# Kernel tuning notes

Hardware: AMD Instinct MI355X
Metric: run time of the kernel (lower is better)

The kernel has to match this reference:

```python
import jax, jax.numpy as jnp
import numpy as np


def setup_inputs() -> dict:
    key = jax.random.key(0)
    k1, k2 = jax.random.split(key)
    B, T, D = 8, 2048, 2048
    layer_in = jax.random.normal(k1, (B, T, D), dtype=jnp.float32)
    # nn.Linear(2D, 2D): weight [out=2D, in=2D], bias [2D]
    W_gate = jax.random.normal(k2, (2 * D, 2 * D), dtype=jnp.float32) * 0.02
    b_gate = jnp.zeros((2 * D,), dtype=jnp.float32)
    return {"layer_in": layer_in, "W_gate": W_gate, "b_gate": b_gate}


def reference(layer_in, W_gate, b_gate):
    # Cumulative average: tril(ones)/row_index @ x  ==  cumsum(x)/[1..t]
    t = layer_in.shape[1]
    denom = jnp.arange(1, t + 1, dtype=layer_in.dtype)[:, None]  # (t, 1)
    average_out = jnp.cumsum(layer_in, axis=1) / denom  # (B, t, D)
    # Gating: Linear(2D -> 2D) on concat(x, avg), then chunk into two gates
    gating_in = jnp.concatenate([layer_in, average_out], axis=-1)  # (B, t, 2D)
    gates = jnp.einsum('btk,ok->bto', gating_in, W_gate) + b_gate  # (B, t, 2D)
    input_gate, forget_gate = jnp.split(gates, 2, axis=2)
    gating_out = (jax.nn.sigmoid(input_gate) * layer_in
                  + jax.nn.sigmoid(forget_gate) * average_out)
    return gating_out, average_out
```

## Files before the change

### kernel.cpp

```cpp
#include <hip/hip_runtime.h>
#include <hip/hip_bf16.h>


#define Bb 8
#define Tt 2048
#define Dd 2048
#define Mm (Bb * Tt)
#define Kk 4096
#define NC 32
#define CT 64

typedef __bf16 bf16x8 __attribute__((ext_vector_type(8)));
typedef float f32x4 __attribute__((ext_vector_type(4)));

__device__ __forceinline__ void gload16(const void* g, void* l) {
    __builtin_amdgcn_global_load_lds(
        (const __attribute__((address_space(1))) unsigned int*)g,
        (__attribute__((address_space(3))) unsigned int*)l, 16, 0, 0);
}

__global__ void wconv_kernel(const float* __restrict__ W,
                             unsigned short* __restrict__ Wb, long n) {
    long i = ((long)blockIdx.x * blockDim.x + threadIdx.x) * 4;
    long stride = (long)gridDim.x * blockDim.x * 4;
    for (; i < n; i += stride) {
        float4 v = *(const float4*)(W + i);
        __hip_bfloat16 a = __float2bfloat16(v.x);
        __hip_bfloat16 b = __float2bfloat16(v.y);
        __hip_bfloat16 c = __float2bfloat16(v.z);
        __hip_bfloat16 d = __float2bfloat16(v.w);
        ushort4 u;
        u.x = *(unsigned short*)&a; u.y = *(unsigned short*)&b;
        u.z = *(unsigned short*)&c; u.w = *(unsigned short*)&d;
        *(ushort4*)(Wb + i) = u;
    }
}

__global__ void ksum_kernel(const float* __restrict__ X, float* __restrict__ S,
                            unsigned short* __restrict__ Gin) {
    int d = blockIdx.y * 256 + threadIdx.x;
    int bc = blockIdx.x;
    int b = bc >> 5, c = bc & 31;
    const float* p = X + ((long)(b * Tt + c * CT)) * Dd + d;
    long row = (long)b * Tt + c * CT;
    float s = 0.f;
#pragma unroll 8
    for (int t = 0; t < CT; ++t) {
        float x = p[(long)t * Dd];
        s += x;
        __hip_bfloat16 xb = __float2bfloat16(x);
        Gin[(row + t) * 4096 + d] = *(unsigned short*)&xb;
    }
    S[(long)bc * Dd + d] = s;
}

__global__ void kscan_kernel(const unsigned short* __restrict__ Ginx,
                             const float* __restrict__ S,
                             float* __restrict__ AVG, unsigned short* __restrict__ Gin) {
    int d = blockIdx.y * 256 + threadIdx.x;
    int bc = blockIdx.x;
    int b = bc >> 5, c = bc & 31;
    const float* Sp = S + (long)(b * NC) * Dd + d;
    float run = 0.f;
    for (int cc = 0; cc < c; ++cc) run += Sp[(long)cc * Dd];
    long row = (long)b * Tt + c * CT;
    for (int tt = 0; tt < CT; ++tt) {
        long r = row + tt;
        union { unsigned int u; float f; } cx;
        cx.u = ((unsigned int)Ginx[r * 4096 + d]) << 16;
        run += cx.f;
        float av = run / (float)(c * CT + tt + 1);
        AVG[r * Dd + d] = av;
        __hip_bfloat16 ab = __float2bfloat16(av);
        Gin[r * 4096 + 2048 + d] = *(unsigned short*)&ab;
    }
}

#define MFMA(va, vb, c_) c_ = __builtin_amdgcn_mfma_f32_16x16x32_bf16(va, vb, c_, 0, 0, 0)
#define RD(p_, i_) (*(const bf16x8*)((p_) + (i_) * 1024))
#define SBAR __builtin_amdgcn_s_barrier()
#define SCHB __builtin_amdgcn_sched_barrier(0)
#define LGKM0 do { asm volatile("s_waitcnt lgkmcnt(0)" ::: "memory"); SCHB; } while (0)

#define CL_LO(B0_, B1_, B2_, B3_)                                               \
    __builtin_amdgcn_s_setprio(1);                                              \
    MFMA(aL0,B0_,acc[0][0]); MFMA(aL0,B1_,acc[0][1]); MFMA(aL0,B2_,acc[0][2]); MFMA(aL0,B3_,acc[0][3]); \
    MFMA(aL1,B0_,acc[1][0]); MFMA(aL1,B1_,acc[1][1]); MFMA(aL1,B2_,acc[1][2]); MFMA(aL1,B3_,acc[1][3]); \
    MFMA(aL2,B0_,acc[2][0]); MFMA(aL2,B1_,acc[2][1]); MFMA(aL2,B2_,acc[2][2]); MFMA(aL2,B3_,acc[2][3]); \
    MFMA(aL3,B0_,acc[3][0]); MFMA(aL3,B1_,acc[3][1]); MFMA(aL3,B2_,acc[3][2]); MFMA(aL3,B3_,acc[3][3]); \
    __builtin_amdgcn_s_setprio(0);
#define CL_HI(B0_, B1_, B2_, B3_)                                               \
    __builtin_amdgcn_s_setprio(1);                                              \
    MFMA(aH0,B0_,acc[4][0]); MFMA(aH0,B1_,acc[4][1]); MFMA(aH0,B2_,acc[4][2]); MFMA(aH0,B3_,acc[4][3]); \
    MFMA(aH1,B0_,acc[5][0]); MFMA(aH1,B1_,acc[5][1]); MFMA(aH1,B2_,acc[5][2]); MFMA(aH1,B3_,acc[5][3]); \
    MFMA(aH2,B0_,acc[6][0]); MFMA(aH2,B1_,acc[6][1]); MFMA(aH2,B2_,acc[6][2]); MFMA(aH2,B3_,acc[6][3]); \
    MFMA(aH3,B0_,acc[7][0]); MFMA(aH3,B1_,acc[7][1]); MFMA(aH3,B2_,acc[7][2]); MFMA(aH3,B3_,acc[7][3]); \
    __builtin_amdgcn_s_setprio(0);

#define TILE64(t_, bb_, STG_, VB_)                                              \
  {                                                                             \
    const char* pa_ = rA0 + (bb_);                                              \
    const char* pb_ = rB0 + (bb_);                                              \
    char* nb_ = ldsb + ((bb_) ^ 65536) + woff;                                  \
    const long ko_ = ((long)(t_) + 1) * 128;                                    \
                                \
    aL0 = RD(pa_,0); aL1 = RD(pa_,1); aL2 = RD(pa_,2); aL3 = RD(pa_,3);         \
    bb0 = RD(pb_,0); bb1 = RD(pb_,1); bb2 = RD(pb_,2); bb3 = RD(pb_,3);         \
    if (STG_) { gload16(gA0 + ko_, nb_); gload16(gA1 + ko_, nb_ + 8192); }      \
    LGKM0;                                                         \
                                      \
    aH0 = RD(pa_,4); aH1 = RD(pa_,5); aH2 = RD(pa_,6); aH3 = RD(pa_,7);         \
    SCHB;                                                                       \
    CL_LO(bb0, bb1, bb2, bb3)                                                   \
    SCHB;                                                                       \
    LGKM0;                                                         \
             \
    aL0 = RD(pa_+32768,0); aL1 = RD(pa_+32768,1); aL2 = RD(pa_+32768,2); aL3 = RD(pa_+32768,3); \
    bd0 = RD(pb_+32768,0); bd1 = RD(pb_+32768,1); bd2 = RD(pb_+32768,2); bd3 = RD(pb_+32768,3); \
    if (STG_) { gload16(gB0 + ko_, nb_ + 16384); gload16(gB1 + ko_, nb_ + 24576); } \
    SCHB;                                                                       \
    CL_HI(bb0, bb1, bb2, bb3)                                                   \
    SCHB;                                                                       \
    LGKM0;                                                         \
                     \
    aH0 = RD(pa_+32768,4); aH1 = RD(pa_+32768,5); aH2 = RD(pa_+32768,6); aH3 = RD(pa_+32768,7); \
    if (STG_) { gload16(gA0 + ko_ + 64, nb_ + 32768); gload16(gA1 + ko_ + 64, nb_ + 40960); } \
    SCHB;                                                                       \
    CL_LO(bd0, bd1, bd2, bd3)                                                   \
    SCHB;                                                                       \
    LGKM0;                                                         \
                                         \
    if (STG_) { gload16(gB0 + ko_ + 64, nb_ + 49152); gload16(gB1 + ko_ + 64, nb_ + 57344); } \
    SCHB;                                                                       \
    CL_HI(bd0, bd1, bd2, bd3)                                                   \
    SCHB;                                                                       \
    asm volatile("s_waitcnt vmcnt(" #VB_ ")" ::: "memory");                     \
    SBAR; SCHB;                                          \
  }

__global__ __launch_bounds__(512, 1) void gemmcf_kernel(
    const unsigned short* __restrict__ Gin,
    const unsigned short* __restrict__ Wb,
    const float* __restrict__ bias,
    float* __restrict__ OUT)
{
    __shared__ __attribute__((aligned(128))) char lds[131072];
    char* ldsb = (char*)lds;

    const int tid = threadIdx.x;
    const int w = tid >> 6, l = tid & 63;
    const int wm = w >> 2, wn = w & 3;
    const int lm = l & 15;
    const int woff = w * 1024;

    const int bid = blockIdx.x;
    const int batch = bid >> 8;
    const int rr = bid & 255;
    const int xcd = rr & 7;
    const int j = rr >> 3;
    const int nt = xcd * 2 + (j >> 4);
    const int mt = batch * 16 + (j & 15);
    const long m0 = (long)mt * 256;
    const int n0 = nt * 128;

    const int srow = tid >> 2;
    const int schunk = (tid & 3) ^ ((tid >> 3) & 3);
    const char* gA0 = (const char*)Gin + (m0 + srow) * 8192 + schunk * 16;
    const char* gA1 = gA0 + 128 * 8192;
    const long jr0 = n0 + ((srow >> 6) << 5) + (srow & 31) + (((srow >> 5) & 1) << 11);
    const int j1 = 128 + srow;
    const long jr1 = n0 + ((j1 >> 6) << 5) + (j1 & 31) + (((j1 >> 5) & 1) << 11);
    const char* gB0 = (const char*)Wb + jr0 * 8192 + schunk * 16;
    const char* gB1 = (const char*)Wb + jr1 * 8192 + schunk * 16;

    const int cbyte = (((l >> 4) ^ ((lm >> 1) & 3))) * 16;
    const char* rA0 = ldsb + (wm * 128 + lm) * 64 + cbyte;
    const char* rB0 = ldsb + 16384 + (wn * 64 + lm) * 64 + cbyte;

    f32x4 acc[8][4] = {};

    bf16x8 aL0, aL1, aL2, aL3, aH0, aH1, aH2, aH3;
    bf16x8 bb0, bb1, bb2, bb3, bd0, bd1, bd2, bd3;

    gload16(gA0,      ldsb + woff);
    gload16(gA1,      ldsb + 8192 + woff);
    gload16(gB0,      ldsb + 16384 + woff);
    gload16(gB1,      ldsb + 24576 + woff);
    gload16(gA0 + 64, ldsb + 32768 + woff);
    gload16(gA1 + 64, ldsb + 40960 + woff);
    gload16(gB0 + 64, ldsb + 49152 + woff);
    gload16(gB1 + 64, ldsb + 57344 + woff);
    asm volatile("s_waitcnt vmcnt(0)" ::: "memory");
    SBAR; SCHB;

#pragma unroll 1
    for (int t = 0; t < 62; t += 2) {
        TILE64(t,     0,     1, 0)
        TILE64(t + 1, 65536, 1, 0)
    }
    TILE64(62, 0,     1, 0)
    TILE64(63, 65536, 0, 0)

#pragma unroll
    for (int mi = 0; mi < 8; ++mi) {
        long rbase = m0 + wm * 128 + mi * 16 + (l >> 4) * 4;
#pragma unroll
        for (int nj = 0; nj < 2; ++nj) {
            int d = n0 + wn * 32 + nj * 16 + lm;
            float bi_ = bias[d];
            float bf_ = bias[d + 2048];
#pragma unroll
            for (int r = 0; r < 4; ++r) {
                long row = rbase + r;
                unsigned int ux = Gin[row * 4096 + d];
                unsigned int ua = Gin[row * 4096 + 2048 + d];
                union { unsigned int u; float f; } cx, ca;
                cx.u = ux << 16; ca.u = ua << 16;
                float gi = acc[mi][nj][r] + bi_;
                float gf = acc[mi][nj + 2][r] + bf_;
                float si = 1.f / (1.f + __expf(-gi));
                float sf = 1.f / (1.f + __expf(-gf));
                OUT[row * 2048 + d] = si * cx.f + sf * ca.f;
            }
        }
    }
}

extern "C" void kernel_launch(void* const* d_in, const int* in_sizes, int n_in,
                              void* d_out, int out_size, void* d_ws, size_t ws_size,
                              hipStream_t stream) {
    const float* X = (const float*)d_in[0];
    const float* W = (const float*)d_in[1];
    const float* bias = (const float*)d_in[2];

    float* OUT = (float*)d_out;
    float* AVG = OUT + (long)Mm * Dd;

    char* ws = (char*)d_ws;
    unsigned short* Wb  = (unsigned short*)ws;
    unsigned short* Gin = (unsigned short*)(ws + 33554432);
    float* S = (float*)(ws + 33554432 + 134217728);

    wconv_kernel<<<2048, 256, 0, stream>>>(W, Wb, (long)Kk * Kk);
    ksum_kernel<<<dim3(Bb * NC, Dd / 256), 256, 0, stream>>>(X, S, Gin);
    kscan_kernel<<<dim3(Bb * NC, Dd / 256), 256, 0, stream>>>(Gin, S, AVG, Gin);
    gemmcf_kernel<<<1024, 512, 0, stream>>>(Gin, Wb, bias, OUT);
}
```

Baseline: 617.1 us.

## Restructure GEMM main loop into five-stage LDS ring with cross-slot register prefetch

Replaces the double-buffered 128-wide K tile loop with a five-slot ring of 32-wide K stages in a larger LDS allocation (160 KB), prefetching three stages ahead. Each slot issues the global-to-LDS loads for a future stage and reads the next slot's A/B fragments into alternating register sets during the current MFMAs. This deepens the memory pipeline and hides LDS-read latency across slots. The cost is more barriers per unit of K work, a more intricate hand-unrolled schedule, and LDS use near the per-CU limit.

```diff
diff --git a/kernel.cpp b/kernel.cpp
--- a/kernel.cpp
+++ b/kernel.cpp
@@ -97,54 +97,45 @@
     MFMA(aH3,B0_,acc[7][0]); MFMA(aH3,B1_,acc[7][1]); MFMA(aH3,B2_,acc[7][2]); MFMA(aH3,B3_,acc[7][3]); \
     __builtin_amdgcn_s_setprio(0);
 
-#define TILE64(t_, bb_, STG_, VB_)                                              \
+#define SLOT(sOFF_, snOFF_, stOFF_, t4_, B0_,B1_,B2_,B3_, N0_,N1_,N2_,N3_, STG_, RDX_, VN_) \
   {                                                                             \
-    const char* pa_ = rA0 + (bb_);                                              \
-    const char* pb_ = rB0 + (bb_);                                              \
-    char* nb_ = ldsb + ((bb_) ^ 65536) + woff;                                  \
-    const long ko_ = ((long)(t_) + 1) * 128;                                    \
-                                \
-    aL0 = RD(pa_,0); aL1 = RD(pa_,1); aL2 = RD(pa_,2); aL3 = RD(pa_,3);         \
-    bb0 = RD(pb_,0); bb1 = RD(pb_,1); bb2 = RD(pb_,2); bb3 = RD(pb_,3);         \
-    if (STG_) { gload16(gA0 + ko_, nb_); gload16(gA1 + ko_, nb_ + 8192); }      \
-    LGKM0;                                                         \
-                                      \
+    const char* pa_ = rA0 + (sOFF_);                                            \
+    const char* qa_ = rA0 + (snOFF_);                                           \
+    const char* qb_ = rB0 + (snOFF_);                                           \
+    char* st_ = ldsb + (stOFF_) + woff;                                         \
+    const long ko_ = (long)(t4_) * 64;                                          \
+    LGKM0;                                          \
     aH0 = RD(pa_,4); aH1 = RD(pa_,5); aH2 = RD(pa_,6); aH3 = RD(pa_,7);         \
-    SCHB;                                                                       \
-    CL_LO(bb0, bb1, bb2, bb3)                                                   \
-    SCHB;                                                                       \
-    LGKM0;                                                         \
-             \
-    aL0 = RD(pa_+32768,0); aL1 = RD(pa_+32768,1); aL2 = RD(pa_+32768,2); aL3 = RD(pa_+32768,3); \
-    bd0 = RD(pb_+32768,0); bd1 = RD(pb_+32768,1); bd2 = RD(pb_+32768,2); bd3 = RD(pb_+32768,3); \
-    if (STG_) { gload16(gB0 + ko_, nb_ + 16384); gload16(gB1 + ko_, nb_ + 24576); } \
-    SCHB;                                                                       \
-    CL_HI(bb0, bb1, bb2, bb3)                                                   \
-    SCHB;                                                                       \
-    LGKM0;                                                         \
-                     \
-    aH0 = RD(pa_+32768,4); aH1 = RD(pa_+32768,5); aH2 = RD(pa_+32768,6); aH3 = RD(pa_+32768,7); \
-    if (STG_) { gload16(gA0 + ko_ + 64, nb_ + 32768); gload16(gA1 + ko_ + 64, nb_ + 40960); } \
-    SCHB;                                                                       \
-    CL_LO(bd0, bd1, bd2, bd3)                                                   \
-    SCHB;                                                                       \
-    LGKM0;                                                         \
-                                         \
-    if (STG_) { gload16(gB0 + ko_ + 64, nb_ + 49152); gload16(gB1 + ko_ + 64, nb_ + 57344); } \
-    SCHB;                                                                       \
-    CL_HI(bd0, bd1, bd2, bd3)                                                   \
-    SCHB;                                                                       \
-    asm volatile("s_waitcnt vmcnt(" #VB_ ")" ::: "memory");                     \
-    SBAR; SCHB;                                          \
+    if (STG_) { gload16(gA0 + ko_, st_); gload16(gA1 + ko_, st_ + 8192); }      \
+    SCHB;                                                                       \
+    CL_LO(B0_, B1_, B2_, B3_)                                                   \
+    SCHB;                                                                       \
+    LGKM0;                                                      \
+    if (RDX_) {                                                                 \
+      aL0 = RD(qa_,0); aL1 = RD(qa_,1); aL2 = RD(qa_,2); aL3 = RD(qa_,3);       \
+      N0_ = RD(qb_,0); N1_ = RD(qb_,1); N2_ = RD(qb_,2); N3_ = RD(qb_,3);       \
+    }                                                                           \
+    if (STG_) { gload16(gB0 + ko_, st_ + 16384); gload16(gB1 + ko_, st_ + 24576); } \
+    SCHB;                                                                       \
+    CL_HI(B0_, B1_, B2_, B3_)                                                   \
+    SCHB;                                                                       \
+    asm volatile("s_waitcnt vmcnt(" #VN_ ")" ::: "memory");                     \
+    SBAR; SCHB;                                                                 \
   }
 
-__global__ __launch_bounds__(512, 1) void gemmcf_kernel(
+#define S0 0
+#define S1 32768
+#define S2 65536
+#define S3 98304
+#define S4 131072
+
+__global__ __launch_bounds__(512, 1) void gemm5r_kernel(
     const unsigned short* __restrict__ Gin,
     const unsigned short* __restrict__ Wb,
     const float* __restrict__ bias,
     float* __restrict__ OUT)
 {
-    __shared__ __attribute__((aligned(128))) char lds[131072];
+    __shared__ __attribute__((aligned(128))) char lds[163840];
     char* ldsb = (char*)lds;
 
     const int tid = threadIdx.x;
@@ -182,24 +173,49 @@
     bf16x8 aL0, aL1, aL2, aL3, aH0, aH1, aH2, aH3;
     bf16x8 bb0, bb1, bb2, bb3, bd0, bd1, bd2, bd3;
 
-    gload16(gA0,      ldsb + woff);
-    gload16(gA1,      ldsb + 8192 + woff);
-    gload16(gB0,      ldsb + 16384 + woff);
-    gload16(gB1,      ldsb + 24576 + woff);
-    gload16(gA0 + 64, ldsb + 32768 + woff);
-    gload16(gA1 + 64, ldsb + 40960 + woff);
-    gload16(gB0 + 64, ldsb + 49152 + woff);
-    gload16(gB1 + 64, ldsb + 57344 + woff);
-    asm volatile("s_waitcnt vmcnt(0)" ::: "memory");
+    gload16(gA0,       ldsb + S0 + woff);
+    gload16(gA1,       ldsb + S0 + 8192 + woff);
+    gload16(gB0,       ldsb + S0 + 16384 + woff);
+    gload16(gB1,       ldsb + S0 + 24576 + woff);
+    gload16(gA0 + 64,  ldsb + S1 + woff);
+    gload16(gA1 + 64,  ldsb + S1 + 8192 + woff);
+    gload16(gB0 + 64,  ldsb + S1 + 16384 + woff);
+    gload16(gB1 + 64,  ldsb + S1 + 24576 + woff);
+    gload16(gA0 + 128, ldsb + S2 + woff);
+    gload16(gA1 + 128, ldsb + S2 + 8192 + woff);
+    gload16(gB0 + 128, ldsb + S2 + 16384 + woff);
+    gload16(gB1 + 128, ldsb + S2 + 24576 + woff);
+    gload16(gA0 + 192, ldsb + S3 + woff);
+    gload16(gA1 + 192, ldsb + S3 + 8192 + woff);
+    gload16(gB0 + 192, ldsb + S3 + 16384 + woff);
+    gload16(gB1 + 192, ldsb + S3 + 24576 + woff);
+    asm volatile("s_waitcnt vmcnt(8)" ::: "memory");
     SBAR; SCHB;
+    aL0 = RD(rA0,0); aL1 = RD(rA0,1); aL2 = RD(rA0,2); aL3 = RD(rA0,3);
+    bb0 = RD(rB0,0); bb1 = RD(rB0,1); bb2 = RD(rB0,2); bb3 = RD(rB0,3);
+    SCHB;
 
 #pragma unroll 1
-    for (int t = 0; t < 62; t += 2) {
-        TILE64(t,     0,     1, 0)
-        TILE64(t + 1, 65536, 1, 0)
-    }
-    TILE64(62, 0,     1, 0)
-    TILE64(63, 65536, 0, 0)
+    for (int t = 0; t < 120; t += 10) {
+        SLOT(S0,S1,S4, t+4,  bb0,bb1,bb2,bb3, bd0,bd1,bd2,bd3, 1,1,8)
+        SLOT(S1,S2,S0, t+5,  bd0,bd1,bd2,bd3, bb0,bb1,bb2,bb3, 1,1,8)
+        SLOT(S2,S3,S1, t+6,  bb0,bb1,bb2,bb3, bd0,bd1,bd2,bd3, 1,1,8)
+        SLOT(S3,S4,S2, t+7,  bd0,bd1,bd2,bd3, bb0,bb1,bb2,bb3, 1,1,8)
+        SLOT(S4,S0,S3, t+8,  bb0,bb1,bb2,bb3, bd0,bd1,bd2,bd3, 1,1,8)
+        SLOT(S0,S1,S4, t+9,  bd0,bd1,bd2,bd3, bb0,bb1,bb2,bb3, 1,1,8)
+        SLOT(S1,S2,S0, t+10, bb0,bb1,bb2,bb3, bd0,bd1,bd2,bd3, 1,1,8)
+        SLOT(S2,S3,S1, t+11, bd0,bd1,bd2,bd3, bb0,bb1,bb2,bb3, 1,1,8)
+        SLOT(S3,S4,S2, t+12, bb0,bb1,bb2,bb3, bd0,bd1,bd2,bd3, 1,1,8)
+        SLOT(S4,S0,S3, t+13, bd0,bd1,bd2,bd3, bb0,bb1,bb2,bb3, 1,1,8)
+    }
+    SLOT(S0,S1,S4, 124, bb0,bb1,bb2,bb3, bd0,bd1,bd2,bd3, 1,1,8)
+    SLOT(S1,S2,S0, 125, bd0,bd1,bd2,bd3, bb0,bb1,bb2,bb3, 1,1,8)
+    SLOT(S2,S3,S1, 126, bb0,bb1,bb2,bb3, bd0,bd1,bd2,bd3, 1,1,8)
+    SLOT(S3,S4,S2, 127, bd0,bd1,bd2,bd3, bb0,bb1,bb2,bb3, 1,1,8)
+    SLOT(S4,S0,S3, 0,   bb0,bb1,bb2,bb3, bd0,bd1,bd2,bd3, 0,1,4)
+    SLOT(S0,S1,S4, 0,   bd0,bd1,bd2,bd3, bb0,bb1,bb2,bb3, 0,1,0)
+    SLOT(S1,S2,S0, 0,   bb0,bb1,bb2,bb3, bd0,bd1,bd2,bd3, 0,1,0)
+    SLOT(S2,S3,S1, 0,   bd0,bd1,bd2,bd3, bb0,bb1,bb2,bb3, 0,0,0)
 
 #pragma unroll
     for (int mi = 0; mi < 8; ++mi) {
@@ -244,5 +260,5 @@
     wconv_kernel<<<2048, 256, 0, stream>>>(W, Wb, (long)Kk * Kk);
     ksum_kernel<<<dim3(Bb * NC, Dd / 256), 256, 0, stream>>>(X, S, Gin);
     kscan_kernel<<<dim3(Bb * NC, Dd / 256), 256, 0, stream>>>(Gin, S, AVG, Gin);
-    gemmcf_kernel<<<1024, 512, 0, stream>>>(Gin, Wb, bias, OUT);
-}
+    gemm5r_kernel<<<1024, 512, 0, stream>>>(Gin, Wb, bias, OUT);
+}
```

Result: faster. 594.6 us, median of 2 (-3.6%).
